# Kernel optimization log

Measured on AMD Instinct MI355X. Metric: run time of the kernel, lower is better.

## Reference

```python
import jax, jax.numpy as jnp
import numpy as np

SIGMA_DIS = 3.0  # from __init__ default sigma_dis=3
PRED_SCALE = 3e-6  # keep sqrt-norms below sigma so max(sigma - d, 0) is not saturated at 0


def setup_inputs() -> dict:
    key = jax.random.key(0)
    k1, k2 = jax.random.split(key)
    C, H, W = 8, 2048, 2048
    K = 32  # number of connected kernel components (labels 1..K, 0 = background)
    pred = jax.random.normal(k1, (C, H, W), dtype=jnp.float32) * PRED_SCALE
    kernel_labels = jax.random.randint(k2, (H, W), 0, K + 1, dtype=jnp.int32)
    regions_mask = jnp.ones((H, W), dtype=bool)  # unused by the original forward
    return {
        "pred_similarities": pred,
        "regions_mask": regions_mask,
        "kernel_labels": kernel_labels,
        "num_kernel": K,
    }


def _l_dis(pred, labels_flat, num_kernel, sigma):
    # pred: [C, H, W]; labels_flat: [H*W] int, values in 0..num_kernel (0 = background).
    C = pred.shape[0]
    flat = pred.reshape(C, -1).T  # [P, C]
    # Per-kernel, per-channel masked sums (the Gk broadcast values): S[k, c]
    S = jax.ops.segment_sum(flat, labels_flat, num_segments=num_kernel + 1)  # [K+1, C]
    # Per-kernel pixel counts N[k]
    N = jax.ops.segment_sum(jnp.ones_like(labels_flat, dtype=pred.dtype),
                            labels_flat, num_segments=num_kernel + 1)  # [K+1]
    # Gk_i has value S[i,c] on kernel i's pixels and 0 elsewhere; supports of distinct
    # kernels are disjoint, so ||Gk_i - Gk_j||_F^2 = N[i]*sum_c S[i,c]^2 + N[j]*sum_c S[j,c]^2.
    A = (N * jnp.sum(S * S, axis=1))[1:]  # [K], drop background label 0
    pair_sq = A[:, None] + A[None, :]  # [K, K]
    D = jnp.maximum(sigma - jnp.sqrt(pair_sq), 0.0)
    term = jnp.log(D * D + 1.0)
    upper = jnp.triu(jnp.ones((num_kernel, num_kernel), dtype=bool), k=1)  # i<j pairs
    L = jnp.sum(jnp.where(upper, term, 0.0))
    scale = (num_kernel - 1) / num_kernel  # 1.0/num_kernel * (num_kernel - 1)
    return L * jnp.asarray(scale, pred.dtype)


def reference(pred_similarities, regions_mask, kernel_labels, num_kernel):
    # regions_mask is accepted but unused, matching the original forward.
    labels_flat = kernel_labels.reshape(-1)
    return _l_dis(pred_similarities, labels_flat, num_kernel, SIGMA_DIS)
```

## Files before the change

### kernel.cpp

```cpp
#include <hip/hip_runtime.h>
#include <hip/hip_bf16.h>
#include <math.h>


typedef __attribute__((ext_vector_type(8))) short short8;
typedef __attribute__((ext_vector_type(4))) float f32x4;

constexpr int NSEGF = 32;
constexpr int RPS   = 9;
constexpr int NROWS = NSEGF * RPS;
constexpr int BLK   = 256;
constexpr int WPB   = 4;
constexpr int NBLK  = 1024;
constexpr int NWAVE = NBLK * WPB;
constexpr int PXS   = 32;
constexpr int L1BLK = 32;
constexpr int SLABS = NBLK / L1BLK;
constexpr int L1BASE   = 1024;
constexpr int PARTBASE = 16384;

#define SCHED_FENCE asm volatile("" ::: "memory")

__device__ __forceinline__ short f2bf(float f) {
  return (short)__bfloat16_as_ushort(__float2bfloat16(f));
}

__device__ __forceinline__ float wave_sum64(float x) {
  int t;
  t = __builtin_amdgcn_update_dpp(0, __float_as_int(x), 0x111, 0xf, 0xf, true); x += __int_as_float(t);
  t = __builtin_amdgcn_update_dpp(0, __float_as_int(x), 0x112, 0xf, 0xf, true); x += __int_as_float(t);
  t = __builtin_amdgcn_update_dpp(0, __float_as_int(x), 0x114, 0xf, 0xf, true); x += __int_as_float(t);
  t = __builtin_amdgcn_update_dpp(0, __float_as_int(x), 0x118, 0xf, 0xf, true); x += __int_as_float(t);
  t = __builtin_amdgcn_update_dpp(0, __float_as_int(x), 0x142, 0xf, 0xf, true); x += __int_as_float(t);
  t = __builtin_amdgcn_update_dpp(0, __float_as_int(x), 0x143, 0xf, 0xf, true); x += __int_as_float(t);
  return x;
}

#define LOADSET(PA, PB, LA, LB, KIDX)                                          \
  {                                                                            \
    int kc_ = (KIDX); if (kc_ > lastk) kc_ = lastk;                            \
    const size_t off_ = (size_t)kc_ * PXS;                                     \
    if (isch) {                                                                \
      PA = *(const float4*)(pc + off_);                                        \
      PB = *(const float4*)(pc + off_ + 4);                                    \
    }                                                                          \
    LA = *(const int4*)(lp + off_);                                            \
    LB = *(const int4*)(lp + off_ + 4);                                        \
  }

#define COMPSET(PA, PB, LA, LB)                                                \
  {                                                                            \
    short8 A0_, A1_, B_;                                                       \
    A0_[0] = (LA.x == ms0) ? ONE : (short)0;                                   \
    A0_[1] = (LA.y == ms0) ? ONE : (short)0;                                   \
    A0_[2] = (LA.z == ms0) ? ONE : (short)0;                                   \
    A0_[3] = (LA.w == ms0) ? ONE : (short)0;                                   \
    A0_[4] = (LB.x == ms0) ? ONE : (short)0;                                   \
    A0_[5] = (LB.y == ms0) ? ONE : (short)0;                                   \
    A0_[6] = (LB.z == ms0) ? ONE : (short)0;                                   \
    A0_[7] = (LB.w == ms0) ? ONE : (short)0;                                   \
    A1_[0] = (LA.x == ms1) ? ONE : (short)0;                                   \
    A1_[1] = (LA.y == ms1) ? ONE : (short)0;                                   \
    A1_[2] = (LA.z == ms1) ? ONE : (short)0;                                   \
    A1_[3] = (LA.w == ms1) ? ONE : (short)0;                                   \
    A1_[4] = (LB.x == ms1) ? ONE : (short)0;                                   \
    A1_[5] = (LB.y == ms1) ? ONE : (short)0;                                   \
    A1_[6] = (LB.z == ms1) ? ONE : (short)0;                                   \
    A1_[7] = (LB.w == ms1) ? ONE : (short)0;                                   \
    if (isch) {                                                                \
      B_[0] = f2bf(PA.x); B_[1] = f2bf(PA.y);                                  \
      B_[2] = f2bf(PA.z); B_[3] = f2bf(PA.w);                                  \
      B_[4] = f2bf(PB.x); B_[5] = f2bf(PB.y);                                  \
      B_[6] = f2bf(PB.z); B_[7] = f2bf(PB.w);                                  \
    } else {                                                                   \
      B_ = Bconst;                                                             \
    }                                                                          \
    acc0 = __builtin_amdgcn_mfma_f32_16x16x32_bf16(A0_, B_, acc0, 0, 0, 0);    \
    acc1 = __builtin_amdgcn_mfma_f32_16x16x32_bf16(A1_, B_, acc1, 0, 0, 0);    \
  }

__global__ __launch_bounds__(BLK, 4)
void seg_mfma(const float* __restrict__ pred,
              const int*   __restrict__ lab,
              float*       __restrict__ ws,
              int P) {
  __shared__ float red[WPB][NROWS];
  const int tid  = threadIdx.x;
  const int wid  = tid >> 6;
  const int lane = tid & 63;
  const int colq = lane & 15;
  const int quad = lane >> 4;
  const int ms0  = colq + 1;
  const int ms1  = colq + 17;
  const short ONE = (short)0x3F80;

  const int bs = (blockIdx.x & 7) * (NBLK / 8) + (blockIdx.x >> 3);
  const int gw = bs * WPB + wid;

  const int nsteps = P / PXS;
  const int spw    = nsteps / NWAVE;
  const int kbase  = gw * spw;
  const int lastk  = nsteps - 1;
  const bool isch  = (colq < 8);
  const float* pc = pred + (size_t)(colq & 7) * P + quad * 8;
  const int*   lp = lab + quad * 8;

  f32x4 acc0 = {0.f, 0.f, 0.f, 0.f};
  f32x4 acc1 = {0.f, 0.f, 0.f, 0.f};

  short8 Bconst;
  {
    const short v = (colq == 8) ? ONE : (short)0;
#pragma unroll
    for (int i = 0; i < 8; ++i) Bconst[i] = v;
  }

  float4 pa0 = {}, pb0 = {}, pa1 = {}, pb1 = {};
  float4 pa2 = {}, pb2 = {}, pa3 = {}, pb3 = {};
  int4   la0, lb0, la1, lb1, la2, lb2, la3, lb3;

  int k = kbase;
  LOADSET(pa0, pb0, la0, lb0, k)
  LOADSET(pa1, pb1, la1, lb1, k + 1)
  LOADSET(pa2, pb2, la2, lb2, k + 2)
  LOADSET(pa3, pb3, la3, lb3, k + 3)

  for (int i = 0; i < spw; i += 4) {
    SCHED_FENCE;
    COMPSET(pa0, pb0, la0, lb0)
    LOADSET(pa0, pb0, la0, lb0, k + 4)
    SCHED_FENCE;
    COMPSET(pa1, pb1, la1, lb1)
    LOADSET(pa1, pb1, la1, lb1, k + 5)
    SCHED_FENCE;
    COMPSET(pa2, pb2, la2, lb2)
    LOADSET(pa2, pb2, la2, lb2, k + 6)
    SCHED_FENCE;
    COMPSET(pa3, pb3, la3, lb3)
    LOADSET(pa3, pb3, la3, lb3, k + 7)
    k += 4;
  }

  if (colq < RPS) {
#pragma unroll
    for (int r = 0; r < 4; ++r)
      red[wid][(quad * 4 + r) * RPS + colq] = acc0[r];
#pragma unroll
    for (int r = 0; r < 4; ++r)
      red[wid][(16 + quad * 4 + r) * RPS + colq] = acc1[r];
  }
  __syncthreads();
  for (int v = tid; v < NROWS; v += BLK) {
    float s = 0.f;
#pragma unroll
    for (int w = 0; w < WPB; ++w) s += red[w][v];
    ws[PARTBASE + (size_t)blockIdx.x * NROWS + v] = s;
  }
}

__global__ __launch_bounds__(256)
void reduce1(float* __restrict__ ws) {
  const int b = blockIdx.x;
  for (int v = threadIdx.x; v < NROWS; v += 256) {
    float s = 0.f;
#pragma unroll 4
    for (int i = 0; i < SLABS; ++i)
      s += ws[PARTBASE + (size_t)(b * SLABS + i) * NROWS + v];
    ws[L1BASE + (size_t)v * L1BLK + b] = s;
  }
}

__global__ __launch_bounds__(BLK)
void seg_gen(const float* __restrict__ pred,
             const int*   __restrict__ lab,
             float*       __restrict__ ws,
             int P, int C) {
  __shared__ float bins[(NSEGF + 1) * RPS];
  const int tid = threadIdx.x;
  for (int i = tid; i < (NSEGF + 1) * RPS; i += BLK) bins[i] = 0.f;
  __syncthreads();
  const int stride = gridDim.x * BLK;
  const int Cc = C < 8 ? C : 8;
  for (int p = blockIdx.x * BLK + tid; p < P; p += stride) {
    int lb = lab[p]; if (lb < 0) lb = 0; if (lb > NSEGF) lb = NSEGF;
    const int o = lb * RPS;
    unsafeAtomicAdd(&bins[o + 8], 1.f);
    for (int c = 0; c < Cc; ++c)
      unsafeAtomicAdd(&bins[o + c], pred[(size_t)c * P + p]);
  }
  __syncthreads();
  for (int i = tid; i < NROWS; i += BLK)
    ws[PARTBASE + (size_t)blockIdx.x * NROWS + i] = bins[RPS + i];
}

__global__ __launch_bounds__(256)
void finish_kernel(const float* __restrict__ ws,
                   const int*   __restrict__ nkp,
                   float*       __restrict__ out,
                   int C) {
  __shared__ float sfin[NROWS];
  __shared__ float sA[NSEGF + 1];
  __shared__ float wsum[4];
  int K = *nkp; if (K > NSEGF) K = NSEGF;
  const int tid = threadIdx.x;
  const int Cc = C < 8 ? C : 8;

  for (int v = tid; v < NROWS; v += 256) {
    const float* r = ws + L1BASE + (size_t)v * L1BLK;
    float s = 0.f;
#pragma unroll
    for (int b = 0; b < L1BLK; ++b) s += r[b];
    sfin[v] = s;
  }
  __syncthreads();
  for (int k = 1 + tid; k <= K; k += 256) {
    float s2 = 0.f;
    for (int c = 0; c < Cc; ++c) {
      const float v = sfin[(k - 1) * RPS + c];
      s2 = fmaf(v, v, s2);
    }
    sA[k] = sfin[(k - 1) * RPS + 8] * s2;
  }
  __syncthreads();

  const int npairs = K * (K - 1) / 2;
  float accv = 0.f;
  for (int idx = tid; idx < npairs; idx += 256) {
    int i = 1, rem = idx;
    while (rem >= K - i) { rem -= K - i; ++i; }
    const int j = i + 1 + rem;
    const float ps = sA[i] + sA[j];
    const float d  = fmaxf(3.0f - sqrtf(ps), 0.f);
    accv += logf(fmaf(d, d, 1.f));
  }
  accv = wave_sum64(accv);
  if ((tid & 63) == 63) wsum[tid >> 6] = accv;
  __syncthreads();
  if (tid == 0)
    out[0] = (wsum[0] + wsum[1] + wsum[2] + wsum[3]) * (float)(K - 1) / (float)K;
}

extern "C" void kernel_launch(void* const* d_in, const int* in_sizes, int n_in,
                              void* d_out, int out_size, void* d_ws, size_t ws_size,
                              hipStream_t stream) {
  const float* pred = (const float*)d_in[0];
  const int*   lab  = (const int*)d_in[2];
  const int*   nkp  = (const int*)d_in[3];
  float*       out  = (float*)d_out;
  float*       ws   = (float*)d_ws;

  const int P = in_sizes[2];
  const int C = in_sizes[0] / P;

  const size_t need = (size_t)(PARTBASE + (size_t)NBLK * NROWS) * sizeof(float);
  const int spw = (P / PXS) / NWAVE;
  const bool fast = (C == 8) && (P % (PXS * NWAVE)) == 0 &&
                    spw >= 4 && (spw & 3) == 0 && ws_size >= need;

  if (fast) {
    seg_mfma<<<NBLK, BLK, 0, stream>>>(pred, lab, ws, P);
  } else {
    seg_gen<<<NBLK, BLK, 0, stream>>>(pred, lab, ws, P, C);
  }
  reduce1<<<L1BLK, 256, 0, stream>>>(ws);
  finish_kernel<<<1, 256, 0, stream>>>(ws, nkp, out, C);
}
```

Baseline: 45.71 us.

## Fuse partial reduction and finish into main kernel via atomic last-block pattern

After: 134.4 us. 2.94x slower.

```diff
diff --git a/kernel.cpp b/kernel.cpp
--- a/kernel.cpp
+++ b/kernel.cpp
@@ -14,10 +14,8 @@
 constexpr int NBLK  = 1024;
 constexpr int NWAVE = NBLK * WPB;
 constexpr int PXS   = 32;
-constexpr int L1BLK = 32;
-constexpr int SLABS = NBLK / L1BLK;
-constexpr int L1BASE   = 1024;
-constexpr int PARTBASE = 16384;
+constexpr int NGRP  = 32;
+constexpr int L1BASE = 256;
 
 #define SCHED_FENCE asm volatile("" ::: "memory")
 
@@ -34,6 +32,67 @@
   t = __builtin_amdgcn_update_dpp(0, __float_as_int(x), 0x142, 0xf, 0xf, true); x += __int_as_float(t);
   t = __builtin_amdgcn_update_dpp(0, __float_as_int(x), 0x143, 0xf, 0xf, true); x += __int_as_float(t);
   return x;
+}
+
+__device__ __forceinline__ void finish_inblock(const float* __restrict__ ws,
+                                               const int*   __restrict__ nkp,
+                                               float*       __restrict__ out,
+                                               int Cc, int tid) {
+  __shared__ float sfin[NROWS];
+  __shared__ float sA[NSEGF + 1];
+  __shared__ float wsum[4];
+  int K = *nkp; if (K > NSEGF) K = NSEGF;
+
+  for (int v = tid; v < NROWS; v += BLK) {
+    const float* r = ws + L1BASE + (size_t)v * NGRP;
+    float s = 0.f;
+#pragma unroll
+    for (int b = 0; b < NGRP; ++b) s += r[b];
+    sfin[v] = s;
+  }
+  __syncthreads();
+  for (int k = 1 + tid; k <= K; k += BLK) {
+    float s2 = 0.f;
+    for (int c = 0; c < Cc; ++c) {
+      const float v = sfin[(k - 1) * RPS + c];
+      s2 = fmaf(v, v, s2);
+    }
+    sA[k] = sfin[(k - 1) * RPS + 8] * s2;
+  }
+  __syncthreads();
+
+  const int npairs = K * (K - 1) / 2;
+  float accv = 0.f;
+  for (int idx = tid; idx < npairs; idx += BLK) {
+    int i = 1, rem = idx;
+    while (rem >= K - i) { rem -= K - i; ++i; }
+    const int j = i + 1 + rem;
+    const float ps = sA[i] + sA[j];
+    const float d  = fmaxf(3.0f - sqrtf(ps), 0.f);
+    accv += logf(fmaf(d, d, 1.f));
+  }
+  accv = wave_sum64(accv);
+  if ((tid & 63) == 63) wsum[tid >> 6] = accv;
+  __syncthreads();
+  if (tid == 0)
+    out[0] = (wsum[0] + wsum[1] + wsum[2] + wsum[3]) * (float)(K - 1) / (float)K;
+}
+
+__device__ __forceinline__ bool publish_and_check_last(float* __restrict__ ws,
+                                                       const float* __restrict__ part,
+                                                       int grp, int tid, int nblk) {
+  for (int v = tid; v < NROWS; v += BLK)
+    unsafeAtomicAdd(&ws[L1BASE + (size_t)v * NGRP + grp], part[v]);
+  __threadfence();
+  __shared__ int lastflag;
+  if (tid == 0) {
+    const int old = atomicAdd((int*)ws, 1);
+    lastflag = (old == nblk - 1);
+  }
+  __syncthreads();
+  if (!lastflag) return false;
+  __threadfence();
+  return true;
 }
 
 #define LOADSET(PA, PB, LA, LB, KIDX)                                          \
@@ -80,11 +139,14 @@
   }
 
 __global__ __launch_bounds__(BLK, 4)
-void seg_mfma(const float* __restrict__ pred,
-              const int*   __restrict__ lab,
-              float*       __restrict__ ws,
-              int P) {
+void seg_mfma_fused(const float* __restrict__ pred,
+                    const int*   __restrict__ lab,
+                    const int*   __restrict__ nkp,
+                    float*       __restrict__ out,
+                    float*       __restrict__ ws,
+                    int P) {
   __shared__ float red[WPB][NROWS];
+  __shared__ float part[NROWS];
   const int tid  = threadIdx.x;
   const int wid  = tid >> 6;
   const int lane = tid & 63;
@@ -154,27 +216,21 @@
     float s = 0.f;
 #pragma unroll
     for (int w = 0; w < WPB; ++w) s += red[w][v];
-    ws[PARTBASE + (size_t)blockIdx.x * NROWS + v] = s;
-  }
-}
-
-__global__ __launch_bounds__(256)
-void reduce1(float* __restrict__ ws) {
-  const int b = blockIdx.x;
-  for (int v = threadIdx.x; v < NROWS; v += 256) {
-    float s = 0.f;
-#pragma unroll 4
-    for (int i = 0; i < SLABS; ++i)
-      s += ws[PARTBASE + (size_t)(b * SLABS + i) * NROWS + v];
-    ws[L1BASE + (size_t)v * L1BLK + b] = s;
-  }
+    part[v] = s;
+  }
+  __syncthreads();
+
+  if (publish_and_check_last(ws, part, blockIdx.x & (NGRP - 1), tid, NBLK))
+    finish_inblock(ws, nkp, out, 8, tid);
 }
 
 __global__ __launch_bounds__(BLK)
-void seg_gen(const float* __restrict__ pred,
-             const int*   __restrict__ lab,
-             float*       __restrict__ ws,
-             int P, int C) {
+void seg_gen_fused(const float* __restrict__ pred,
+                   const int*   __restrict__ lab,
+                   const int*   __restrict__ nkp,
+                   float*       __restrict__ out,
+                   float*       __restrict__ ws,
+                   int P, int C) {
   __shared__ float bins[(NSEGF + 1) * RPS];
   const int tid = threadIdx.x;
   for (int i = tid; i < (NSEGF + 1) * RPS; i += BLK) bins[i] = 0.f;
@@ -189,55 +245,10 @@
       unsafeAtomicAdd(&bins[o + c], pred[(size_t)c * P + p]);
   }
   __syncthreads();
-  for (int i = tid; i < NROWS; i += BLK)
-    ws[PARTBASE + (size_t)blockIdx.x * NROWS + i] = bins[RPS + i];
-}
-
-__global__ __launch_bounds__(256)
-void finish_kernel(const float* __restrict__ ws,
-                   const int*   __restrict__ nkp,
-                   float*       __restrict__ out,
-                   int C) {
-  __shared__ float sfin[NROWS];
-  __shared__ float sA[NSEGF + 1];
-  __shared__ float wsum[4];
-  int K = *nkp; if (K > NSEGF) K = NSEGF;
-  const int tid = threadIdx.x;
-  const int Cc = C < 8 ? C : 8;
-
-  for (int v = tid; v < NROWS; v += 256) {
-    const float* r = ws + L1BASE + (size_t)v * L1BLK;
-    float s = 0.f;
-#pragma unroll
-    for (int b = 0; b < L1BLK; ++b) s += r[b];
-    sfin[v] = s;
-  }
-  __syncthreads();
-  for (int k = 1 + tid; k <= K; k += 256) {
-    float s2 = 0.f;
-    for (int c = 0; c < Cc; ++c) {
-      const float v = sfin[(k - 1) * RPS + c];
-      s2 = fmaf(v, v, s2);
-    }
-    sA[k] = sfin[(k - 1) * RPS + 8] * s2;
-  }
-  __syncthreads();
-
-  const int npairs = K * (K - 1) / 2;
-  float accv = 0.f;
-  for (int idx = tid; idx < npairs; idx += 256) {
-    int i = 1, rem = idx;
-    while (rem >= K - i) { rem -= K - i; ++i; }
-    const int j = i + 1 + rem;
-    const float ps = sA[i] + sA[j];
-    const float d  = fmaxf(3.0f - sqrtf(ps), 0.f);
-    accv += logf(fmaf(d, d, 1.f));
-  }
-  accv = wave_sum64(accv);
-  if ((tid & 63) == 63) wsum[tid >> 6] = accv;
-  __syncthreads();
-  if (tid == 0)
-    out[0] = (wsum[0] + wsum[1] + wsum[2] + wsum[3]) * (float)(K - 1) / (float)K;
+
+  if (publish_and_check_last(ws, bins + RPS, blockIdx.x & (NGRP - 1), tid,
+                             (int)gridDim.x))
+    finish_inblock(ws, nkp, out, Cc, tid);
 }
 
 extern "C" void kernel_launch(void* const* d_in, const int* in_sizes, int n_in,
@@ -252,16 +263,15 @@
   const int P = in_sizes[2];
   const int C = in_sizes[0] / P;
 
-  const size_t need = (size_t)(PARTBASE + (size_t)NBLK * NROWS) * sizeof(float);
+  hipMemsetAsync(d_ws, 0, (size_t)(L1BASE + NROWS * NGRP) * sizeof(float), stream);
+
   const int spw = (P / PXS) / NWAVE;
   const bool fast = (C == 8) && (P % (PXS * NWAVE)) == 0 &&
-                    spw >= 4 && (spw & 3) == 0 && ws_size >= need;
+                    spw >= 4 && (spw & 3) == 0;
 
   if (fast) {
-    seg_mfma<<<NBLK, BLK, 0, stream>>>(pred, lab, ws, P);
+    seg_mfma_fused<<<NBLK, BLK, 0, stream>>>(pred, lab, nkp, out, ws, P);
   } else {
-    seg_gen<<<NBLK, BLK, 0, stream>>>(pred, lab, ws, P, C);
-  }
-  reduce1<<<L1BLK, 256, 0, stream>>>(ws);
-  finish_kernel<<<1, 256, 0, stream>>>(ws, nkp, out, C);
-}
+    seg_gen_fused<<<NBLK, BLK, 0, stream>>>(pred, lab, nkp, out, ws, P, C);
+  }
+}
```
